# Kernel tuning notes

Measured on AMD Instinct MI355X. Metric: run time of the kernel, lower is better.

The kernel has to match this reference:

```python
import jax, jax.numpy as jnp
import numpy as np

N_NODES = 100000
N_EDGES = 1280000
N_PAIRS = 500000
IN_CH = 64
HID = 64
OUT_CH = 1


def setup_inputs() -> dict:
    key = jax.random.key(0)
    ks = jax.random.split(key, 16)
    s = lambda fan_in: 1.0 / np.sqrt(fan_in)
    return {
        "x": jax.random.normal(ks[0], (N_NODES, IN_CH), dtype=jnp.float32),
        "edge_index": jax.random.randint(ks[1], (2, N_EDGES), 0, N_NODES, dtype=jnp.int32),
        "edge_pairs": jax.random.randint(ks[2], (N_PAIRS, 2), 0, N_NODES, dtype=jnp.int32),
        "W1l": jax.random.normal(ks[3], (IN_CH, HID), dtype=jnp.float32) * s(IN_CH),
        "b1l": jnp.zeros((HID,), dtype=jnp.float32),
        "W1r": jax.random.normal(ks[4], (IN_CH, HID), dtype=jnp.float32) * s(IN_CH),
        "W2l": jax.random.normal(ks[5], (HID, HID), dtype=jnp.float32) * s(HID),
        "b2l": jnp.zeros((HID,), dtype=jnp.float32),
        "W2r": jax.random.normal(ks[6], (HID, HID), dtype=jnp.float32) * s(HID),
        "Wr1": jax.random.normal(ks[7], (2 * HID, 64), dtype=jnp.float32) * s(2 * HID),
        "br1": jnp.zeros((64,), dtype=jnp.float32),
        "Wr2": jax.random.normal(ks[8], (64, OUT_CH), dtype=jnp.float32) * s(64),
        "br2": jnp.zeros((OUT_CH,), dtype=jnp.float32),
    }


def sage_conv(x, src, dst, Wl, bl, Wr, num_nodes):
    # PyG SAGEConv (aggr='mean'): out = lin_l(mean_{j in N(i)} x_j) + lin_r(x_i)
    msg = x[src]                                            # [E, C] gather
    agg = jax.ops.segment_sum(msg, dst, num_segments=num_nodes)  # [N, C]
    cnt = jax.ops.segment_sum(jnp.ones_like(dst, dtype=x.dtype), dst,
                              num_segments=num_nodes)       # [N]
    mean = agg / jnp.maximum(cnt, 1.0)[:, None]             # nodes w/o neighbors -> 0
    return mean @ Wl + bl + x @ Wr


def reference(x, edge_index, edge_pairs, W1l, b1l, W1r, W2l, b2l, W2r,
              Wr1, br1, Wr2, br2):
    n = x.shape[0]
    src, dst = edge_index[0], edge_index[1]
    h = jax.nn.relu(sage_conv(x, src, dst, W1l, b1l, W1r, n))
    h = jax.nn.relu(sage_conv(h, src, dst, W2l, b2l, W2r, n))
    h_pair = jnp.concatenate([h[edge_pairs[:, 0]], h[edge_pairs[:, 1]]], axis=1)  # [P, 2H]
    return jax.nn.relu(h_pair @ Wr1 + br1) @ Wr2 + br2
```

## Files before the change

### kernel.cpp

```cpp
#include <hip/hip_runtime.h>
#include <stdint.h>

#define N_NODES 100000
#define N_EDGES 1280000
#define N_PAIRS 500000
#define ELL_STRIDE 48
#define FILL_PASSES 2

typedef _Float16 half_t;
typedef __attribute__((ext_vector_type(8))) _Float16 half8;
typedef __attribute__((ext_vector_type(4))) float f32x4;

union H8U { half8 h; int u[4]; };

__global__ void init_all_kernel(int* __restrict__ cursor, int* __restrict__ adj,
                                int* __restrict__ zrow, int zoff, int N,
                                const float* __restrict__ W1l, const float* __restrict__ W1r,
                                const float* __restrict__ W2l, const float* __restrict__ W2r,
                                const float* __restrict__ Wr1, half_t* __restrict__ Bt) {
  int t = blockIdx.x * blockDim.x + threadIdx.x;
  if (t < N) cursor[t] = 0;
  if (t < 32) zrow[t] = 0;
  if (t < N * 4) {
    int node = t >> 2, q = t & 3;
    *(int4*)&adj[(size_t)node * ELL_STRIDE + q * 4] = make_int4(zoff, zoff, zoff, zoff);
  }
  if (t < 3 * 128 * 64) {
    int g = t >> 13, rem = t & 8191;
    int n = rem >> 6, k = rem & 63;
    const float* B;
    if (g == 0) B = (n < 64) ? W1l : W1r;
    else if (g == 1) B = (n < 64) ? W2l : W2r;
    else B = (n < 64) ? Wr1 : (Wr1 + 64 * 64);
    Bt[t] = (half_t)B[k * 64 + (n & 63)];
  }
}

__global__ void fill_ell_kernel(const int* __restrict__ src, const int* __restrict__ dst,
                                int* __restrict__ cursor, int* __restrict__ adj, int E,
                                int lo, int hi) {
  int t = blockIdx.x * blockDim.x + threadIdx.x;
  if (t < E) {
    int d = dst[t];
    if (d >= lo && d < hi) {
      int pos = atomicAdd(&cursor[d], 1);
      if (pos < ELL_STRIDE) adj[(size_t)d * ELL_STRIDE + pos] = src[t] << 7;
    }
  }
}

template <bool AHALF>
__global__ __launch_bounds__(256) void gemm_mfma(
    const void* __restrict__ Av, const half_t* __restrict__ Bt,
    half_t* __restrict__ C1, half_t* __restrict__ C2, int M) {
  const int tid = threadIdx.x;
  const int wave = tid >> 6, l = tid & 63;
  const int lr = l & 15;
  const int kg = l >> 4;
  const int m_base = blockIdx.x * 128 + wave * 32;

  half8 a[2][2];
  #pragma unroll
  for (int mt = 0; mt < 2; ++mt) {
    int row = m_base + mt * 16 + lr;
    row = min(row, M - 1);
    if (AHALF) {
      const half_t* A = (const half_t*)Av;
      #pragma unroll
      for (int ks = 0; ks < 2; ++ks)
        a[mt][ks] = *(const half8*)&A[(size_t)row * 64 + ks * 32 + kg * 8];
    } else {
      const float* A = (const float*)Av;
      #pragma unroll
      for (int ks = 0; ks < 2; ++ks) {
        float4 f0 = *(const float4*)&A[(size_t)row * 64 + ks * 32 + kg * 8];
        float4 f1 = *(const float4*)&A[(size_t)row * 64 + ks * 32 + kg * 8 + 4];
        half8 h;
        h[0] = (half_t)f0.x; h[1] = (half_t)f0.y; h[2] = (half_t)f0.z; h[3] = (half_t)f0.w;
        h[4] = (half_t)f1.x; h[5] = (half_t)f1.y; h[6] = (half_t)f1.z; h[7] = (half_t)f1.w;
        a[mt][ks] = h;
      }
    }
  }

  f32x4 acc[2][8];
  #pragma unroll
  for (int mt = 0; mt < 2; ++mt)
    #pragma unroll
    for (int nt = 0; nt < 8; ++nt) acc[mt][nt] = (f32x4)(0.f);

  #pragma unroll
  for (int nt = 0; nt < 8; ++nt) {
    half8 b0 = *(const half8*)&Bt[(size_t)(nt * 16 + lr) * 64 + kg * 8];
    half8 b1 = *(const half8*)&Bt[(size_t)(nt * 16 + lr) * 64 + 32 + kg * 8];
    #pragma unroll
    for (int mt = 0; mt < 2; ++mt) {
      acc[mt][nt] = __builtin_amdgcn_mfma_f32_16x16x32_f16(a[mt][0], b0, acc[mt][nt], 0, 0, 0);
      acc[mt][nt] = __builtin_amdgcn_mfma_f32_16x16x32_f16(a[mt][1], b1, acc[mt][nt], 0, 0, 0);
    }
  }

  #pragma unroll
  for (int mt = 0; mt < 2; ++mt) {
    #pragma unroll
    for (int r = 0; r < 4; ++r) {
      int row = m_base + mt * 16 + kg * 4 + r;
      if (row < M) {
        #pragma unroll
        for (int nt = 0; nt < 4; ++nt)
          C1[(size_t)row * 64 + nt * 16 + lr] = (half_t)acc[mt][nt][r];
        #pragma unroll
        for (int nt = 4; nt < 8; ++nt)
          C2[(size_t)row * 64 + (nt - 4) * 16 + lr] = (half_t)acc[mt][nt][r];
      }
    }
  }
}

__global__ __launch_bounds__(256) void agg_kernel(
    const half_t* __restrict__ Qh, const half_t* __restrict__ Pt,
    const int* __restrict__ cnt, const int* __restrict__ adj,
    const float* __restrict__ bias, half_t* __restrict__ Hh, int N) {
  int lane = threadIdx.x & 63;
  int node = blockIdx.x * 8 + ((threadIdx.x >> 6) << 1) + (lane >> 5);
  if (node >= N) return;
  int sub = lane & 31;
  int g = sub >> 3;
  int cb = (sub & 7) * 8;
  const int4* arow4 = (const int4*)(adj + (size_t)node * ELL_STRIDE);
  const int ZOFF = N * 128;
  const char* Qb = (const char*)Qh + cb * 2;

  int4 q0 = arow4[g];
  int4 q1 = arow4[4 + g];
  int deg = cnt[node];
  half8 ph = *(const half8*)&Pt[(size_t)node * 64 + cb];

  half8 w0 = *(const half8*)(Qb + q0.x);
  half8 w1 = *(const half8*)(Qb + q0.y);
  half8 w2 = *(const half8*)(Qb + q0.z);
  half8 w3 = *(const half8*)(Qb + q0.w);
  w0 += w1; w2 += w3;

  H8U a;
  a.h = w0 + w2;

  if (deg > 16) {
    int m = min(deg, ELL_STRIDE);
    int s1 = 16 + g * 4;
    int o4 = (s1 + 0 < m) ? q1.x : ZOFF;
    int o5 = (s1 + 1 < m) ? q1.y : ZOFF;
    int o6 = (s1 + 2 < m) ? q1.z : ZOFF;
    int o7 = (s1 + 3 < m) ? q1.w : ZOFF;
    half8 w4 = *(const half8*)(Qb + o4);
    half8 w5 = *(const half8*)(Qb + o5);
    half8 w6 = *(const half8*)(Qb + o6);
    half8 w7 = *(const half8*)(Qb + o7);
    w4 += w5; w6 += w7;
    a.h += w4 + w6;

    if (deg > 32) {
      int4 q2 = arow4[8 + g];
      int s2 = 32 + g * 4;
      int t0 = (s2 + 0 < m) ? q2.x : ZOFF;
      int t1 = (s2 + 1 < m) ? q2.y : ZOFF;
      int t2 = (s2 + 2 < m) ? q2.z : ZOFF;
      int t3 = (s2 + 3 < m) ? q2.w : ZOFF;
      half8 u0 = *(const half8*)(Qb + t0);
      half8 u1 = *(const half8*)(Qb + t1);
      half8 u2 = *(const half8*)(Qb + t2);
      half8 u3 = *(const half8*)(Qb + t3);
      u0 += u1; u2 += u3;
      a.h += u0 + u2;
    }
  }

  {
    H8U b;
    #pragma unroll
    for (int k = 0; k < 4; ++k) b.u[k] = __shfl_down(a.u[k], 8);
    a.h += b.h;
    #pragma unroll
    for (int k = 0; k < 4; ++k) b.u[k] = __shfl_down(a.u[k], 16);
    a.h += b.h;
  }

  if (sub < 8) {
    float inv = 1.f / fmaxf((float)deg, 1.f);
    float4 ba = *(const float4*)&bias[cb];
    float4 bb = *(const float4*)&bias[cb + 4];
    float bs[8] = {ba.x, ba.y, ba.z, ba.w, bb.x, bb.y, bb.z, bb.w};
    half8 o;
    #pragma unroll
    for (int i = 0; i < 8; ++i) {
      float v = (float)a.h[i] * inv + (float)ph[i] + bs[i];
      o[i] = (half_t)fmaxf(v, 0.f);
    }
    *(half8*)&Hh[(size_t)node * 64 + cb] = o;
  }
}

__global__ __launch_bounds__(256) void pair_kernel(
    const half_t* __restrict__ Uh, const half_t* __restrict__ Vh, const int* __restrict__ pairs,
    const float* __restrict__ br1, const float* __restrict__ Wr2, const float* __restrict__ br2,
    float* __restrict__ out, int P) {
  int wave = blockIdx.x * 4 + (threadIdx.x >> 6);
  int lane = threadIdx.x & 63;
  int h = lane >> 4;
  int sub = lane & 15;
  int side = sub >> 3;
  int cb = (sub & 7) * 8;
  int pA = wave * 8 + h;
  int pB = pA + 4;
  if (pA >= P) return;

  int2 prA = *(const int2*)&pairs[2 * pA];
  int2 prB = (pB < P) ? *(const int2*)&pairs[2 * pB] : prA;
  int nodeA = side ? prA.y : prA.x;
  int nodeB = side ? prB.y : prB.x;
  const half_t* T = side ? Vh : Uh;
  H8U a, c;
  a.h = *(const half8*)&T[(size_t)nodeA * 64 + cb];
  c.h = *(const half8*)&T[(size_t)nodeB * 64 + cb];

  H8U b;
  #pragma unroll
  for (int k = 0; k < 4; ++k) b.u[k] = __shfl_down(a.u[k], 8);
  a.h += b.h;
  #pragma unroll
  for (int k = 0; k < 4; ++k) b.u[k] = __shfl_down(c.u[k], 8);
  c.h += b.h;

  float4 b0 = *(const float4*)&br1[cb];
  float4 b1 = *(const float4*)&br1[cb + 4];
  float4 w0 = *(const float4*)&Wr2[cb];
  float4 w1 = *(const float4*)&Wr2[cb + 4];

  float rA = 0.f, rB = 0.f;
  if (side == 0) {
    rA = fmaxf((float)a.h[0] + b0.x, 0.f) * w0.x + fmaxf((float)a.h[1] + b0.y, 0.f) * w0.y
       + fmaxf((float)a.h[2] + b0.z, 0.f) * w0.z + fmaxf((float)a.h[3] + b0.w, 0.f) * w0.w
       + fmaxf((float)a.h[4] + b1.x, 0.f) * w1.x + fmaxf((float)a.h[5] + b1.y, 0.f) * w1.y
       + fmaxf((float)a.h[6] + b1.z, 0.f) * w1.z + fmaxf((float)a.h[7] + b1.w, 0.f) * w1.w;
    rB = fmaxf((float)c.h[0] + b0.x, 0.f) * w0.x + fmaxf((float)c.h[1] + b0.y, 0.f) * w0.y
       + fmaxf((float)c.h[2] + b0.z, 0.f) * w0.z + fmaxf((float)c.h[3] + b0.w, 0.f) * w0.w
       + fmaxf((float)c.h[4] + b1.x, 0.f) * w1.x + fmaxf((float)c.h[5] + b1.y, 0.f) * w1.y
       + fmaxf((float)c.h[6] + b1.z, 0.f) * w1.z + fmaxf((float)c.h[7] + b1.w, 0.f) * w1.w;
  }
  rA += __shfl_xor(rA, 1);
  rA += __shfl_xor(rA, 2);
  rA += __shfl_xor(rA, 4);
  rB += __shfl_xor(rB, 1);
  rB += __shfl_xor(rB, 2);
  rB += __shfl_xor(rB, 4);
  if (sub == 0) {
    out[pA] = rA + br2[0];
    if (pB < P) out[pB] = rB + br2[0];
  }
}

extern "C" void kernel_launch(void* const* d_in, const int* in_sizes, int n_in,
                              void* d_out, int out_size, void* d_ws, size_t ws_size,
                              hipStream_t stream) {
  const float* x   = (const float*)d_in[0];
  const int*   ei  = (const int*)d_in[1];
  const int* pairs = (const int*)d_in[2];
  const float* W1l = (const float*)d_in[3];
  const float* b1l = (const float*)d_in[4];
  const float* W1r = (const float*)d_in[5];
  const float* W2l = (const float*)d_in[6];
  const float* b2l = (const float*)d_in[7];
  const float* W2r = (const float*)d_in[8];
  const float* Wr1 = (const float*)d_in[9];
  const float* br1 = (const float*)d_in[10];
  const float* Wr2 = (const float*)d_in[11];
  const float* br2 = (const float*)d_in[12];
  float* out = (float*)d_out;

  const int N = N_NODES, E = N_EDGES, P = N_PAIRS;
  const int* srcI = ei;
  const int* dstI = ei + E;

  char* w = (char*)d_ws;
  int* cursor = (int*)w;  w += (size_t)N * 4;
  w = (char*)(((uintptr_t)w + 255) & ~(uintptr_t)255);
  int* adj = (int*)w;     w += (size_t)N * ELL_STRIDE * 4;
  w = (char*)(((uintptr_t)w + 255) & ~(uintptr_t)255);
  half_t* Qh = (half_t*)w; w += (size_t)(N + 1) * 64 * 2;
  w = (char*)(((uintptr_t)w + 255) & ~(uintptr_t)255);
  half_t* Pt = (half_t*)w; w += (size_t)N * 64 * 2;
  w = (char*)(((uintptr_t)w + 255) & ~(uintptr_t)255);
  half_t* Hh = (half_t*)w; w += (size_t)N * 64 * 2;
  w = (char*)(((uintptr_t)w + 255) & ~(uintptr_t)255);
  half_t* Bt = (half_t*)w; w += (size_t)3 * 128 * 64 * 2;
  half_t* Vh = Pt;

  init_all_kernel<<<(N * 4 + 255) / 256, 256, 0, stream>>>(
      cursor, adj, (int*)(Qh + (size_t)N * 64), N * 128, N,
      W1l, W1r, W2l, W2r, Wr1, Bt);

  {
    const int EB = (E + 255) / 256;
    const int step = (N + FILL_PASSES - 1) / FILL_PASSES;
    for (int k = 0; k < FILL_PASSES; ++k) {
      int lo = k * step;
      int hi = min(N, lo + step);
      fill_ell_kernel<<<EB, 256, 0, stream>>>(srcI, dstI, cursor, adj, E, lo, hi);
    }
  }

  const int GB = (N + 127) / 128;
  gemm_mfma<false><<<GB, 256, 0, stream>>>((const void*)x, Bt, Qh, Pt, N);
  agg_kernel<<<(N + 7) / 8, 256, 0, stream>>>(Qh, Pt, cursor, adj, b1l, Hh, N);
  gemm_mfma<true><<<GB, 256, 0, stream>>>((const void*)Hh, Bt + 8192, Qh, Pt, N);
  agg_kernel<<<(N + 7) / 8, 256, 0, stream>>>(Qh, Pt, cursor, adj, b2l, Hh, N);
  gemm_mfma<true><<<GB, 256, 0, stream>>>((const void*)Hh, Bt + 16384, Qh, Vh, N);
  pair_kernel<<<(P + 31) / 32, 256, 0, stream>>>(Qh, Vh, pairs, br1, Wr2, br2, out, P);
}
```

Baseline: 218.6 us.

## Partition ELL fill by destination range per XCD in a single launch

Replaces the two-pass ELL fill (two launches, each scanning all edges for half the node range) with one kernel. Blocks are mapped to XCDs via blockIdx & 7, and each XCD handles one eighth of the destination-node range so its atomics and adjacency writes stay in that XCD's L2. Each thread processes 8 edges. This relies on round-robin block-to-XCD dispatch, and every edge is still read by 8 blocks, which multiplies dst reads.

Result: faster. 194.6 us (-11.0%).

```diff
diff --git a/kernel.cpp b/kernel.cpp
--- a/kernel.cpp
+++ b/kernel.cpp
@@ -5,7 +5,8 @@
 #define N_EDGES 1280000
 #define N_PAIRS 500000
 #define ELL_STRIDE 48
-#define FILL_PASSES 2
+#define NXCD 8
+#define EDGES_PER_THREAD 8
 
 typedef _Float16 half_t;
 typedef __attribute__((ext_vector_type(8))) _Float16 half8;
@@ -36,15 +37,23 @@
   }
 }
 
-__global__ void fill_ell_kernel(const int* __restrict__ src, const int* __restrict__ dst,
-                                int* __restrict__ cursor, int* __restrict__ adj, int E,
-                                int lo, int hi) {
-  int t = blockIdx.x * blockDim.x + threadIdx.x;
-  if (t < E) {
-    int d = dst[t];
-    if (d >= lo && d < hi) {
-      int pos = atomicAdd(&cursor[d], 1);
-      if (pos < ELL_STRIDE) adj[(size_t)d * ELL_STRIDE + pos] = src[t] << 7;
+__global__ void fill_xcd_kernel(const int* __restrict__ src, const int* __restrict__ dst,
+                                int* __restrict__ cursor, int* __restrict__ adj, int E) {
+  const int xcd = blockIdx.x & (NXCD - 1);
+  const int chunk = blockIdx.x >> 3;
+  const int step = (N_NODES + NXCD - 1) / NXCD;
+  const int lo = xcd * step;
+  const int hi = min(N_NODES, lo + step);
+  const int base = chunk * (256 * EDGES_PER_THREAD) + threadIdx.x;
+  #pragma unroll
+  for (int i = 0; i < EDGES_PER_THREAD; ++i) {
+    int e = base + i * 256;
+    if (e < E) {
+      int d = dst[e];
+      if (d >= lo && d < hi) {
+        int pos = atomicAdd(&cursor[d], 1);
+        if (pos < ELL_STRIDE) adj[(size_t)d * ELL_STRIDE + pos] = src[e] << 7;
+      }
     }
   }
 }
@@ -300,13 +309,8 @@
       W1l, W1r, W2l, W2r, Wr1, Bt);
 
   {
-    const int EB = (E + 255) / 256;
-    const int step = (N + FILL_PASSES - 1) / FILL_PASSES;
-    for (int k = 0; k < FILL_PASSES; ++k) {
-      int lo = k * step;
-      int hi = min(N, lo + step);
-      fill_ell_kernel<<<EB, 256, 0, stream>>>(srcI, dstI, cursor, adj, E, lo, hi);
-    }
+    const int chunks = (E + 256 * EDGES_PER_THREAD - 1) / (256 * EDGES_PER_THREAD);
+    fill_xcd_kernel<<<chunks * NXCD, 256, 0, stream>>>(srcI, dstI, cursor, adj, E);
   }
 
   const int GB = (N + 127) / 128;
```

## Build ELL adjacency with per-block node windows and shared-memory cursors

Applied to the files above, without the earlier changes.

Replaces the global-atomic two-pass ELL fill with a single kernel of 256 blocks. Each block owns a window of 391 destination nodes, scans the whole dst array, and counts slots with LDS atomics, writing cursors back at the end. The adj padding initialization moves into the same kernel. This removes global atomic contention and a separate init pass, at the cost of every block reading all 1.28M dst entries, about 1.3 GB of total L2 traffic.

New measurement: 434.0 us. 98.5% more time.

```diff
diff --git a/kernel.cpp b/kernel.cpp
--- a/kernel.cpp
+++ b/kernel.cpp
@@ -5,7 +5,8 @@
 #define N_EDGES 1280000
 #define N_PAIRS 500000
 #define ELL_STRIDE 48
-#define FILL_PASSES 2
+#define NWIN 256
+#define WINDOW 391
 
 typedef _Float16 half_t;
 typedef __attribute__((ext_vector_type(8))) _Float16 half8;
@@ -13,18 +14,12 @@
 
 union H8U { half8 h; int u[4]; };
 
-__global__ void init_all_kernel(int* __restrict__ cursor, int* __restrict__ adj,
-                                int* __restrict__ zrow, int zoff, int N,
-                                const float* __restrict__ W1l, const float* __restrict__ W1r,
-                                const float* __restrict__ W2l, const float* __restrict__ W2r,
-                                const float* __restrict__ Wr1, half_t* __restrict__ Bt) {
+__global__ void init_misc_kernel(int* __restrict__ zrow,
+                                 const float* __restrict__ W1l, const float* __restrict__ W1r,
+                                 const float* __restrict__ W2l, const float* __restrict__ W2r,
+                                 const float* __restrict__ Wr1, half_t* __restrict__ Bt) {
   int t = blockIdx.x * blockDim.x + threadIdx.x;
-  if (t < N) cursor[t] = 0;
   if (t < 32) zrow[t] = 0;
-  if (t < N * 4) {
-    int node = t >> 2, q = t & 3;
-    *(int4*)&adj[(size_t)node * ELL_STRIDE + q * 4] = make_int4(zoff, zoff, zoff, zoff);
-  }
   if (t < 3 * 128 * 64) {
     int g = t >> 13, rem = t & 8191;
     int n = rem >> 6, k = rem & 63;
@@ -36,17 +31,38 @@
   }
 }
 
-__global__ void fill_ell_kernel(const int* __restrict__ src, const int* __restrict__ dst,
-                                int* __restrict__ cursor, int* __restrict__ adj, int E,
-                                int lo, int hi) {
-  int t = blockIdx.x * blockDim.x + threadIdx.x;
-  if (t < E) {
-    int d = dst[t];
-    if (d >= lo && d < hi) {
-      int pos = atomicAdd(&cursor[d], 1);
-      if (pos < ELL_STRIDE) adj[(size_t)d * ELL_STRIDE + pos] = src[t] << 7;
-    }
-  }
+__global__ __launch_bounds__(512) void build_kernel(
+    const int* __restrict__ src, const int* __restrict__ dst,
+    int* __restrict__ cursor, int* __restrict__ adj, int zoff) {
+  __shared__ int lcur[WINDOW];
+  const int tid = threadIdx.x;
+  const int lo = blockIdx.x * WINDOW;
+  const int hi = min(N_NODES, lo + WINDOW);
+  const int wn = hi - lo;
+
+  for (int i = tid; i < wn; i += 512) lcur[i] = 0;
+  for (int i = tid; i < wn * 4; i += 512) {
+    int node = lo + (i >> 2), q = i & 3;
+    *(int4*)&adj[(size_t)node * ELL_STRIDE + q * 4] = make_int4(zoff, zoff, zoff, zoff);
+  }
+  __syncthreads();
+
+  #pragma unroll 2
+  for (int it = 0; it < N_EDGES / (512 * 4); ++it) {
+    int e0 = it * 2048 + tid * 4;
+    int4 d4 = *(const int4*)&dst[e0];
+    int dv[4] = {d4.x, d4.y, d4.z, d4.w};
+    #pragma unroll
+    for (int i = 0; i < 4; ++i) {
+      int d = dv[i];
+      if (d >= lo && d < hi) {
+        int pos = atomicAdd(&lcur[d - lo], 1);
+        if (pos < ELL_STRIDE) adj[(size_t)d * ELL_STRIDE + pos] = src[e0 + i] << 7;
+      }
+    }
+  }
+  __syncthreads();
+  for (int i = tid; i < wn; i += 512) cursor[lo + i] = lcur[i];
 }
 
 template <bool AHALF>
@@ -295,19 +311,10 @@
   half_t* Bt = (half_t*)w; w += (size_t)3 * 128 * 64 * 2;
   half_t* Vh = Pt;
 
-  init_all_kernel<<<(N * 4 + 255) / 256, 256, 0, stream>>>(
-      cursor, adj, (int*)(Qh + (size_t)N * 64), N * 128, N,
-      W1l, W1r, W2l, W2r, Wr1, Bt);
-
-  {
-    const int EB = (E + 255) / 256;
-    const int step = (N + FILL_PASSES - 1) / FILL_PASSES;
-    for (int k = 0; k < FILL_PASSES; ++k) {
-      int lo = k * step;
-      int hi = min(N, lo + step);
-      fill_ell_kernel<<<EB, 256, 0, stream>>>(srcI, dstI, cursor, adj, E, lo, hi);
-    }
-  }
+  init_misc_kernel<<<(3 * 128 * 64 + 255) / 256, 256, 0, stream>>>(
+      (int*)(Qh + (size_t)N * 64), W1l, W1r, W2l, W2r, Wr1, Bt);
+
+  build_kernel<<<NWIN, 512, 0, stream>>>(srcI, dstI, cursor, adj, N * 128);
 
   const int GB = (N + 127) / 128;
   gemm_mfma<false><<<GB, 256, 0, stream>>>((const void*)x, Bt, Qh, Pt, N);
```
